# Performance work log

Hardware: AMD Instinct MI355X
Metric: run time of the kernel (lower is better)

The kernel has to match this reference:

```python
import jax, jax.numpy as jnp
import numpy as np

ANGLE_BINS = 16
RADIUS_BINS = 8


def _bilinear_cart(img, ys, xs):
    # img [B,C,H,W]; ys/xs: sample grid [A,R] in pixel coords, zero outside image
    h, w = img.shape[2], img.shape[3]
    y0 = jnp.floor(ys)
    x0 = jnp.floor(xs)
    wy = (ys - y0).astype(img.dtype)
    wx = (xs - x0).astype(img.dtype)
    y0i = jnp.clip(y0, 0, h - 1).astype(jnp.int32)
    y1i = jnp.clip(y0 + 1, 0, h - 1).astype(jnp.int32)
    x0i = jnp.clip(x0, 0, w - 1).astype(jnp.int32)
    x1i = jnp.clip(x0 + 1, 0, w - 1).astype(jnp.int32)
    v00 = img[:, :, y0i, x0i]
    v01 = img[:, :, y0i, x1i]
    v10 = img[:, :, y1i, x0i]
    v11 = img[:, :, y1i, x1i]
    out = (v00 * (1 - wy) * (1 - wx) + v01 * (1 - wy) * wx
           + v10 * wy * (1 - wx) + v11 * wy * wx)
    valid = ((ys >= 0) & (ys <= h - 1) & (xs >= 0) & (xs <= w - 1)).astype(img.dtype)
    return out * valid


def cartesian_to_polar(x):
    # [B,C,H,W] -> [B,C,ANGLE_BINS,RADIUS_BINS] via bilinear sampling on a polar grid
    b, c, h, w = x.shape
    cy = (h - 1) / 2.0
    cx = (w - 1) / 2.0
    max_r = min(h, w) / 2.0
    theta = 2.0 * jnp.pi * jnp.arange(ANGLE_BINS, dtype=jnp.float32) / ANGLE_BINS
    r = (jnp.arange(RADIUS_BINS, dtype=jnp.float32) + 0.5) / RADIUS_BINS * max_r
    ys = cy + r[None, :] * jnp.sin(theta)[:, None]  # [A,R]
    xs = cx + r[None, :] * jnp.cos(theta)[:, None]  # [A,R]
    return _bilinear_cart(x, ys, xs)


def polar_to_cartesian(pf, h, w):
    # [B,C,A,R] -> [B,C,H,W]: inverse remap with angular wrap, radial clamp,
    # zero outside the max radius disc
    b, c, A, R = pf.shape
    cy = (h - 1) / 2.0
    cx = (w - 1) / 2.0
    max_r = min(h, w) / 2.0
    yy, xx = jnp.meshgrid(jnp.arange(h, dtype=jnp.float32),
                          jnp.arange(w, dtype=jnp.float32), indexing='ij')
    dy = yy - cy
    dx = xx - cx
    rr = jnp.sqrt(dy * dy + dx * dx)
    th = jnp.mod(jnp.arctan2(dy, dx), 2.0 * jnp.pi)
    a = th / (2.0 * jnp.pi) * A
    ri = rr / max_r * R - 0.5
    a0 = jnp.floor(a)
    wa = (a - a0).astype(pf.dtype)
    a0i = jnp.mod(a0.astype(jnp.int32), A)
    a1i = jnp.mod(a0i + 1, A)
    r0 = jnp.floor(ri)
    wr = (ri - r0).astype(pf.dtype)
    r0i = jnp.clip(r0, 0, R - 1).astype(jnp.int32)
    r1i = jnp.clip(r0 + 1, 0, R - 1).astype(jnp.int32)
    v00 = pf[:, :, a0i, r0i]
    v01 = pf[:, :, a0i, r1i]
    v10 = pf[:, :, a1i, r0i]
    v11 = pf[:, :, a1i, r1i]
    out = (v00 * (1 - wa) * (1 - wr) + v01 * (1 - wa) * wr
           + v10 * wa * (1 - wr) + v11 * wa * wr)
    valid = (rr <= max_r).astype(pf.dtype)
    return out * valid


def setup_inputs() -> dict:
    key = jax.random.key(0)
    ks = jax.random.split(key, 4)
    B, C, H, W = 16, 256, 128, 128
    x = jax.random.normal(ks[0], (B, C, H, W), dtype=jnp.float32)
    # grouped 3x3 conv: groups=4 -> kernel [C_out=C, C_in/groups=C//4, 3, 3]
    w_polar = jax.random.normal(ks[1], (C, C // 4, 3, 3), dtype=jnp.float32) * 0.05
    b_polar = jnp.zeros((C,), jnp.float32)
    w_attn1 = jax.random.normal(ks[2], (C // 4, C), dtype=jnp.float32) * 0.05
    b_attn1 = jnp.zeros((C // 4,), jnp.float32)
    w_attn2 = jax.random.normal(ks[3], (1, C // 4), dtype=jnp.float32) * 0.05
    b_attn2 = jnp.zeros((1,), jnp.float32)
    return {"x": x, "w_polar": w_polar, "b_polar": b_polar,
            "w_attn1": w_attn1, "b_attn1": b_attn1,
            "w_attn2": w_attn2, "b_attn2": b_attn2}


def reference(x, w_polar, b_polar, w_attn1, b_attn1, w_attn2, b_attn2):
    b, c, h, w = x.shape
    pf = cartesian_to_polar(x)  # [B,C,16,8]
    pp = jax.lax.conv_general_dilated(
        pf, w_polar, window_strides=(1, 1), padding=((1, 1), (1, 1)),
        dimension_numbers=('NCHW', 'OIHW', 'NCHW'), feature_group_count=4)
    pp = pp + b_polar[None, :, None, None]
    pc = polar_to_cartesian(pp, h, w)  # [B,C,H,W]
    h1 = jax.nn.relu(jnp.einsum('bchw,oc->bohw', pc, w_attn1)
                     + b_attn1[None, :, None, None])
    att = jax.nn.sigmoid(jnp.einsum('bchw,oc->bohw', h1, w_attn2)
                         + b_attn2[None, :, None, None])  # [B,1,H,W]
    return x * att
```

## Files before the change

kernel.cpp:

```cpp
#include <hip/hip_runtime.h>
#include <math.h>

#define TWO_PI 6.28318530717958647692f

typedef float f4 __attribute__((ext_vector_type(4)));

__global__ __launch_bounds__(256) void k1_cart2polar(const float* __restrict__ x,
                                                     float* __restrict__ pf) {
    __shared__ float w00s[128], w01s[128], w10s[128], w11s[128];
    __shared__ int   o00s[128], o01s[128], o10s[128], o11s[128];
    int tid = threadIdx.x;
    if (tid < 128) {
        int a = tid >> 3, r = tid & 7;
        float theta = (TWO_PI * (float)a) / 16.0f;
        float rad   = ((float)r + 0.5f) / 8.0f * 64.0f;
        float ys = 63.5f + rad * sinf(theta);
        float xs = 63.5f + rad * cosf(theta);
        float y0 = floorf(ys), x0 = floorf(xs);
        float wy = ys - y0,    wx = xs - x0;
        int y0i = min(max((int)y0, 0), 127);
        int y1i = min(max((int)y0 + 1, 0), 127);
        int x0i = min(max((int)x0, 0), 127);
        int x1i = min(max((int)x0 + 1, 0), 127);
        float valid = (ys >= 0.0f && ys <= 127.0f && xs >= 0.0f && xs <= 127.0f) ? 1.0f : 0.0f;
        w00s[tid] = valid * (1.0f - wy) * (1.0f - wx);
        w01s[tid] = valid * (1.0f - wy) * wx;
        w10s[tid] = valid * wy * (1.0f - wx);
        w11s[tid] = valid * wy * wx;
        o00s[tid] = y0i * 128 + x0i;
        o01s[tid] = y0i * 128 + x1i;
        o10s[tid] = y1i * 128 + x0i;
        o11s[tid] = y1i * 128 + x1i;
    }
    __syncthreads();
    int t = blockIdx.x * 256 + tid;
    int bin = t & 127;
    int img = t >> 7;
    const float* ib = x + ((size_t)img << 14);
    float v = ib[o00s[bin]] * w00s[bin]
            + ib[o01s[bin]] * w01s[bin]
            + ib[o10s[bin]] * w10s[bin]
            + ib[o11s[bin]] * w11s[bin];
    pf[t] = v;
}

__global__ __launch_bounds__(256) void k2_conv(const float* __restrict__ pf,
                                               const float* __restrict__ w_polar,
                                               const float* __restrict__ b_polar,
                                               float* __restrict__ pp_t) {
    __shared__ __align__(16) float pfs[64 * 180];
    __shared__ __align__(16) float red[128 * 8];
    int bid = blockIdx.x;
    int b  = bid >> 5;
    int g  = (bid >> 3) & 3;
    int ot = bid & 7;
    int tid = threadIdx.x;
    for (int i = tid; i < 64 * 180; i += 256) pfs[i] = 0.0f;
    __syncthreads();
    const float* src = pf + ((size_t)(b * 256 + g * 64) << 7);
    for (int i = tid; i < 8192; i += 256) {
        int ic = i >> 7, bin = i & 127;
        pfs[ic * 180 + ((bin >> 3) + 1) * 10 + (bin & 7) + 1] = src[i];
    }
    __syncthreads();

    int half = tid >> 7;
    int bt   = tid & 127;
    int a = bt >> 3, r = bt & 7;
    int oc0 = g * 64 + ot * 8;
    float acc[8];
    #pragma unroll
    for (int j = 0; j < 8; ++j) acc[j] = 0.0f;

    const float* wbase = w_polar + (size_t)oc0 * 576 + half * 288;
    const float* pbase = pfs + half * 32 * 180 + a * 10 + r;
    for (int ic = 0; ic < 32; ++ic) {
        float v[9];
        const float* base = pbase + ic * 180;
        #pragma unroll
        for (int dh = 0; dh < 3; ++dh)
            #pragma unroll
            for (int dw = 0; dw < 3; ++dw)
                v[dh * 3 + dw] = base[dh * 10 + dw];
        #pragma unroll
        for (int j = 0; j < 8; ++j) {
            const float* wp = wbase + j * 576 + ic * 9;
            acc[j] += wp[0]*v[0] + wp[1]*v[1] + wp[2]*v[2]
                    + wp[3]*v[3] + wp[4]*v[4] + wp[5]*v[5]
                    + wp[6]*v[6] + wp[7]*v[7] + wp[8]*v[8];
        }
    }
    if (half) {
        #pragma unroll
        for (int j = 0; j < 8; ++j) red[bt * 8 + j] = acc[j];
    }
    __syncthreads();
    if (!half) {
        float* dst = pp_t + ((size_t)((b << 7) + bt)) * 256 + oc0;
        #pragma unroll
        for (int j = 0; j < 8; ++j)
            dst[j] = acc[j] + red[bt * 8 + j] + b_polar[oc0 + j];
    }
}

__global__ __launch_bounds__(256) void k3_proj(const float* __restrict__ pp_t,
                                               const float* __restrict__ w_attn1,
                                               float* __restrict__ q) {
    __shared__ __align__(16) float wl[16384];
    int tid = threadIdx.x;
    for (int i = tid; i < 16384; i += 256) {
        int o = i >> 8, c = i & 255;
        wl[(c << 6) + (o ^ (c & 31))] = w_attn1[i];
    }
    __syncthreads();
    int n = blockIdx.x * 256 + tid;
    int b   = n >> 13;
    int bin = (n >> 6) & 127;
    int o   = n & 63;
    const float4* pr4 = (const float4*)(pp_t + ((size_t)((b << 7) + bin)) * 256);
    float acc = 0.0f;
    #pragma unroll 8
    for (int c4 = 0; c4 < 64; ++c4) {
        float4 p = pr4[c4];
        int c = c4 << 2;
        acc += wl[( c      << 6) + (o ^ ( c      & 31))] * p.x;
        acc += wl[((c + 1) << 6) + (o ^ ((c + 1) & 31))] * p.y;
        acc += wl[((c + 2) << 6) + (o ^ ((c + 2) & 31))] * p.z;
        acc += wl[((c + 3) << 6) + (o ^ ((c + 3) & 31))] * p.w;
    }
    q[n] = acc;
}

__global__ __launch_bounds__(256) void k4a_att(const float* __restrict__ q,
                                               const float* __restrict__ b_attn1,
                                               const float* __restrict__ w_attn2,
                                               const float* __restrict__ b_attn2,
                                               float* __restrict__ att) {
    __shared__ __align__(16) float qs[8896];
    __shared__ __align__(16) float b1s[64];
    __shared__ __align__(16) float w2s[64];
    int b    = blockIdx.x >> 6;
    int tile = blockIdx.x & 63;
    int tid  = threadIdx.x;
    const float* qb = q + ((size_t)b << 13);
    for (int i = tid; i < 8192; i += 256) {
        int bin = i >> 6, o = i & 63;
        qs[(bin >> 3) * 556 + (bin & 7) * 68 + o] = qb[i];
    }
    if (tid < 64) { b1s[tid] = b_attn1[tid]; w2s[tid] = w_attn2[tid]; }
    __syncthreads();
    float b2 = b_attn2[0];
    const float4* q4  = (const float4*)qs;
    const float4* b14 = (const float4*)b1s;
    const float4* w24 = (const float4*)w2s;

    int p = (tile << 8) + tid;
    int h = p >> 7, w = p & 127;
    float dy = (float)h - 63.5f;
    float dx = (float)w - 63.5f;
    float rr = sqrtf(dy * dy + dx * dx);
    float th = atan2f(dy, dx);
    if (th < 0.0f) th += TWO_PI;
    float aa = th / TWO_PI * 16.0f;
    float a0 = floorf(aa);
    float wa = aa - a0;
    int ia0 = ((int)a0) & 15;
    int ia1 = (ia0 + 1) & 15;
    float ri = rr / 64.0f * 8.0f - 0.5f;
    float r0 = floorf(ri);
    float wr = ri - r0;
    int ir0 = (int)fminf(fmaxf(r0, 0.0f), 7.0f);
    int ir1 = (int)fminf(fmaxf(r0 + 1.0f, 0.0f), 7.0f);
    float valid = (rr <= 64.0f) ? 1.0f : 0.0f;
    float w00 = valid * (1.0f - wa) * (1.0f - wr);
    float w01 = valid * (1.0f - wa) * wr;
    float w10 = valid * wa * (1.0f - wr);
    float w11 = valid * wa * wr;
    int t00 = ia0 * 139 + ir0 * 17;
    int t01 = ia0 * 139 + ir1 * 17;
    int t10 = ia1 * 139 + ir0 * 17;
    int t11 = ia1 * 139 + ir1 * 17;
    float acc = b2;
    #pragma unroll
    for (int i = 0; i < 16; ++i) {
        float4 v00 = q4[t00 + i], v01 = q4[t01 + i];
        float4 v10 = q4[t10 + i], v11 = q4[t11 + i];
        float4 bb = b14[i], ww = w24[i];
        float sx = w00 * v00.x + w01 * v01.x + w10 * v10.x + w11 * v11.x;
        float sy = w00 * v00.y + w01 * v01.y + w10 * v10.y + w11 * v11.y;
        float sz = w00 * v00.z + w01 * v01.z + w10 * v10.z + w11 * v11.z;
        float sw = w00 * v00.w + w01 * v01.w + w10 * v10.w + w11 * v11.w;
        acc += fmaxf(sx + bb.x, 0.0f) * ww.x;
        acc += fmaxf(sy + bb.y, 0.0f) * ww.y;
        acc += fmaxf(sz + bb.z, 0.0f) * ww.z;
        acc += fmaxf(sw + bb.w, 0.0f) * ww.w;
    }
    float attv = 1.0f / (1.0f + __expf(-acc));
    att[((size_t)b << 14) + p] = attv;
}

__global__ __launch_bounds__(256) void k4b_mul(const f4* __restrict__ x4,
                                               const float* __restrict__ att,
                                               f4* __restrict__ out4) {
    const f4* att4 = (const f4*)att;
    int idx = blockIdx.x * 256 + threadIdx.x;
    int stride = gridDim.x * 256;
    for (int i = idx; i < 16777216; i += stride) {
        f4 xv = __builtin_nontemporal_load(&x4[i]);
        f4 av = att4[((i >> 20) << 12) | (i & 4095)];
        __builtin_nontemporal_store(xv * av, &out4[i]);
    }
}

extern "C" void kernel_launch(void* const* d_in, const int* in_sizes, int n_in,
                              void* d_out, int out_size, void* d_ws, size_t ws_size,
                              hipStream_t stream) {
    const float* x       = (const float*)d_in[0];
    const float* w_polar = (const float*)d_in[1];
    const float* b_polar = (const float*)d_in[2];
    const float* w_attn1 = (const float*)d_in[3];
    const float* b_attn1 = (const float*)d_in[4];
    const float* w_attn2 = (const float*)d_in[5];
    const float* b_attn2 = (const float*)d_in[6];
    float* out = (float*)d_out;
    float* ws  = (float*)d_ws;

    float* pf   = ws;
    float* pp_t = ws + 524288;
    float* q    = ws + 1048576;
    float* att  = ws + 1179648;

    hipLaunchKernelGGL(k1_cart2polar, dim3(2048), dim3(256), 0, stream, x, pf);
    hipLaunchKernelGGL(k2_conv,       dim3(512),  dim3(256), 0, stream, pf, w_polar, b_polar, pp_t);
    hipLaunchKernelGGL(k3_proj,       dim3(512),  dim3(256), 0, stream, pp_t, w_attn1, q);
    hipLaunchKernelGGL(k4a_att,       dim3(1024), dim3(256), 0, stream, q, b_attn1, w_attn2, b_attn2, att);
    hipLaunchKernelGGL(k4b_mul,       dim3(4096), dim3(256), 0, stream,
                       (const f4*)x, att, (f4*)out);
}
```

Measured before the change: 176.6 us.

## Fuse all stages into one persistent kernel with software grid barriers

Merges the five stage kernels into a single persistent kernel of 256 blocks. Stages are separated by an atomic-counter grid barrier, and each block covers several of the old blocks' work per stage. The aim is to remove the launch gaps and tail drain between the small kernels. The cost is far fewer resident blocks (256 blocks of 256 threads) for the bandwidth-bound final multiply, plus spin-barrier overhead and a memset. The barrier also relies on all 256 blocks being co-resident, which is not guaranteed without a cooperative launch.

```diff
diff --git a/kernel.cpp b/kernel.cpp
--- a/kernel.cpp
+++ b/kernel.cpp
@@ -5,210 +5,240 @@
 
 typedef float f4 __attribute__((ext_vector_type(4)));
 
-__global__ __launch_bounds__(256) void k1_cart2polar(const float* __restrict__ x,
-                                                     float* __restrict__ pf) {
-    __shared__ float w00s[128], w01s[128], w10s[128], w11s[128];
-    __shared__ int   o00s[128], o01s[128], o10s[128], o11s[128];
+#define NBLK 256u
+
+__device__ __forceinline__ void gbar(unsigned* cnt, unsigned target) {
+    __syncthreads();
+    __threadfence();
+    if (threadIdx.x == 0) {
+        atomicAdd(cnt, 1u);
+        while (__hip_atomic_load(cnt, __ATOMIC_ACQUIRE,
+                                 __HIP_MEMORY_SCOPE_AGENT) < target)
+            __builtin_amdgcn_s_sleep(4);
+    }
+    __syncthreads();
+    __threadfence();
+}
+
+__global__ __launch_bounds__(256, 2) void mega(
+        const float* __restrict__ x,
+        const float* __restrict__ w_polar,
+        const float* __restrict__ b_polar,
+        const float* __restrict__ w_attn1,
+        const float* __restrict__ b_attn1,
+        const float* __restrict__ w_attn2,
+        const float* __restrict__ b_attn2,
+        float* __restrict__ pf,
+        float* __restrict__ pp_t,
+        float* __restrict__ q,
+        float* __restrict__ att,
+        float* __restrict__ out,
+        unsigned* __restrict__ barcnt) {
+    __shared__ __align__(16) float sp[16384];
     int tid = threadIdx.x;
-    if (tid < 128) {
-        int a = tid >> 3, r = tid & 7;
-        float theta = (TWO_PI * (float)a) / 16.0f;
-        float rad   = ((float)r + 0.5f) / 8.0f * 64.0f;
-        float ys = 63.5f + rad * sinf(theta);
-        float xs = 63.5f + rad * cosf(theta);
-        float y0 = floorf(ys), x0 = floorf(xs);
-        float wy = ys - y0,    wx = xs - x0;
-        int y0i = min(max((int)y0, 0), 127);
-        int y1i = min(max((int)y0 + 1, 0), 127);
-        int x0i = min(max((int)x0, 0), 127);
-        int x1i = min(max((int)x0 + 1, 0), 127);
-        float valid = (ys >= 0.0f && ys <= 127.0f && xs >= 0.0f && xs <= 127.0f) ? 1.0f : 0.0f;
-        w00s[tid] = valid * (1.0f - wy) * (1.0f - wx);
-        w01s[tid] = valid * (1.0f - wy) * wx;
-        w10s[tid] = valid * wy * (1.0f - wx);
-        w11s[tid] = valid * wy * wx;
-        o00s[tid] = y0i * 128 + x0i;
-        o01s[tid] = y0i * 128 + x1i;
-        o10s[tid] = y1i * 128 + x0i;
-        o11s[tid] = y1i * 128 + x1i;
-    }
-    __syncthreads();
-    int t = blockIdx.x * 256 + tid;
-    int bin = t & 127;
-    int img = t >> 7;
-    const float* ib = x + ((size_t)img << 14);
-    float v = ib[o00s[bin]] * w00s[bin]
-            + ib[o01s[bin]] * w01s[bin]
-            + ib[o10s[bin]] * w10s[bin]
-            + ib[o11s[bin]] * w11s[bin];
-    pf[t] = v;
-}
-
-__global__ __launch_bounds__(256) void k2_conv(const float* __restrict__ pf,
-                                               const float* __restrict__ w_polar,
-                                               const float* __restrict__ b_polar,
-                                               float* __restrict__ pp_t) {
-    __shared__ __align__(16) float pfs[64 * 180];
-    __shared__ __align__(16) float red[128 * 8];
-    int bid = blockIdx.x;
-    int b  = bid >> 5;
-    int g  = (bid >> 3) & 3;
-    int ot = bid & 7;
-    int tid = threadIdx.x;
-    for (int i = tid; i < 64 * 180; i += 256) pfs[i] = 0.0f;
-    __syncthreads();
-    const float* src = pf + ((size_t)(b * 256 + g * 64) << 7);
-    for (int i = tid; i < 8192; i += 256) {
-        int ic = i >> 7, bin = i & 127;
-        pfs[ic * 180 + ((bin >> 3) + 1) * 10 + (bin & 7) + 1] = src[i];
-    }
-    __syncthreads();
-
-    int half = tid >> 7;
-    int bt   = tid & 127;
-    int a = bt >> 3, r = bt & 7;
-    int oc0 = g * 64 + ot * 8;
-    float acc[8];
-    #pragma unroll
-    for (int j = 0; j < 8; ++j) acc[j] = 0.0f;
-
-    const float* wbase = w_polar + (size_t)oc0 * 576 + half * 288;
-    const float* pbase = pfs + half * 32 * 180 + a * 10 + r;
-    for (int ic = 0; ic < 32; ++ic) {
-        float v[9];
-        const float* base = pbase + ic * 180;
-        #pragma unroll
-        for (int dh = 0; dh < 3; ++dh)
-            #pragma unroll
-            for (int dw = 0; dw < 3; ++dw)
-                v[dh * 3 + dw] = base[dh * 10 + dw];
+    int blk = blockIdx.x;
+
+    {
+        float* w00s = sp;        float* w01s = sp + 128;
+        float* w10s = sp + 256;  float* w11s = sp + 384;
+        int*   o00s = (int*)(sp + 512);  int* o01s = (int*)(sp + 640);
+        int*   o10s = (int*)(sp + 768);  int* o11s = (int*)(sp + 896);
+        if (tid < 128) {
+            int a = tid >> 3, r = tid & 7;
+            float theta = (TWO_PI * (float)a) / 16.0f;
+            float rad   = ((float)r + 0.5f) / 8.0f * 64.0f;
+            float ys = 63.5f + rad * sinf(theta);
+            float xs = 63.5f + rad * cosf(theta);
+            float y0 = floorf(ys), x0 = floorf(xs);
+            float wy = ys - y0,    wx = xs - x0;
+            int y0i = min(max((int)y0, 0), 127);
+            int y1i = min(max((int)y0 + 1, 0), 127);
+            int x0i = min(max((int)x0, 0), 127);
+            int x1i = min(max((int)x0 + 1, 0), 127);
+            float valid = (ys >= 0.0f && ys <= 127.0f && xs >= 0.0f && xs <= 127.0f) ? 1.0f : 0.0f;
+            w00s[tid] = valid * (1.0f - wy) * (1.0f - wx);
+            w01s[tid] = valid * (1.0f - wy) * wx;
+            w10s[tid] = valid * wy * (1.0f - wx);
+            w11s[tid] = valid * wy * wx;
+            o00s[tid] = y0i * 128 + x0i;
+            o01s[tid] = y0i * 128 + x1i;
+            o10s[tid] = y1i * 128 + x0i;
+            o11s[tid] = y1i * 128 + x1i;
+        }
+        __syncthreads();
+        int bin = tid & 127;
+        float W0 = w00s[bin], W1 = w01s[bin], W2 = w10s[bin], W3 = w11s[bin];
+        int O0 = o00s[bin], O1 = o01s[bin], O2 = o10s[bin], O3 = o11s[bin];
         #pragma unroll
         for (int j = 0; j < 8; ++j) {
-            const float* wp = wbase + j * 576 + ic * 9;
-            acc[j] += wp[0]*v[0] + wp[1]*v[1] + wp[2]*v[2]
-                    + wp[3]*v[3] + wp[4]*v[4] + wp[5]*v[5]
-                    + wp[6]*v[6] + wp[7]*v[7] + wp[8]*v[8];
-        }
-    }
-    if (half) {
+            int t = blk * 2048 + j * 256 + tid;
+            int img = t >> 7;
+            const float* ib = x + ((size_t)img << 14);
+            pf[t] = ib[O0] * W0 + ib[O1] * W1 + ib[O2] * W2 + ib[O3] * W3;
+        }
+    }
+    gbar(barcnt, 1 * NBLK);
+
+    {
+        float* pfs = sp;
+        float* red = sp + 11520;
+        for (int i = tid; i < 64 * 180; i += 256) pfs[i] = 0.0f;
+        for (int rep = 0; rep < 2; ++rep) {
+            int role = (blk << 1) | rep;
+            int b  = role >> 5;
+            int g  = (role >> 3) & 3;
+            int ot = role & 7;
+            __syncthreads();
+            const float* src = pf + ((size_t)(b * 256 + g * 64) << 7);
+            for (int i = tid; i < 8192; i += 256) {
+                int ic = i >> 7, bin = i & 127;
+                pfs[ic * 180 + ((bin >> 3) + 1) * 10 + (bin & 7) + 1] = src[i];
+            }
+            __syncthreads();
+            int half = tid >> 7;
+            int bt   = tid & 127;
+            int a = bt >> 3, r = bt & 7;
+            int oc0 = g * 64 + ot * 8;
+            float acc[8];
+            #pragma unroll
+            for (int j = 0; j < 8; ++j) acc[j] = 0.0f;
+            const float* wbase = w_polar + (size_t)oc0 * 576 + half * 288;
+            const float* pbase = pfs + half * 32 * 180 + a * 10 + r;
+            for (int ic = 0; ic < 32; ++ic) {
+                float v[9];
+                const float* base = pbase + ic * 180;
+                #pragma unroll
+                for (int dh = 0; dh < 3; ++dh)
+                    #pragma unroll
+                    for (int dw = 0; dw < 3; ++dw)
+                        v[dh * 3 + dw] = base[dh * 10 + dw];
+                #pragma unroll
+                for (int j = 0; j < 8; ++j) {
+                    const float* wp = wbase + j * 576 + ic * 9;
+                    acc[j] += wp[0]*v[0] + wp[1]*v[1] + wp[2]*v[2]
+                            + wp[3]*v[3] + wp[4]*v[4] + wp[5]*v[5]
+                            + wp[6]*v[6] + wp[7]*v[7] + wp[8]*v[8];
+                }
+            }
+            if (half) {
+                #pragma unroll
+                for (int j = 0; j < 8; ++j) red[bt * 8 + j] = acc[j];
+            }
+            __syncthreads();
+            if (!half) {
+                float* dst = pp_t + ((size_t)((b << 7) + bt)) * 256 + oc0;
+                #pragma unroll
+                for (int j = 0; j < 8; ++j)
+                    dst[j] = acc[j] + red[bt * 8 + j] + b_polar[oc0 + j];
+            }
+        }
+    }
+    gbar(barcnt, 2 * NBLK);
+
+    {
+        float* wl = sp;
+        for (int i = tid; i < 16384; i += 256) {
+            int o = i >> 8, c = i & 255;
+            wl[(c << 6) + (o ^ (c & 31))] = w_attn1[i];
+        }
+        __syncthreads();
         #pragma unroll
-        for (int j = 0; j < 8; ++j) red[bt * 8 + j] = acc[j];
-    }
-    __syncthreads();
-    if (!half) {
-        float* dst = pp_t + ((size_t)((b << 7) + bt)) * 256 + oc0;
+        for (int rep = 0; rep < 2; ++rep) {
+            int n = blk * 512 + rep * 256 + tid;
+            int b   = n >> 13;
+            int bin = (n >> 6) & 127;
+            int o   = n & 63;
+            const float4* pr4 = (const float4*)(pp_t + ((size_t)((b << 7) + bin)) * 256);
+            float acc = 0.0f;
+            #pragma unroll 8
+            for (int c4 = 0; c4 < 64; ++c4) {
+                float4 p = pr4[c4];
+                int c = c4 << 2;
+                acc += wl[( c      << 6) + (o ^ ( c      & 31))] * p.x;
+                acc += wl[((c + 1) << 6) + (o ^ ((c + 1) & 31))] * p.y;
+                acc += wl[((c + 2) << 6) + (o ^ ((c + 2) & 31))] * p.z;
+                acc += wl[((c + 3) << 6) + (o ^ ((c + 3) & 31))] * p.w;
+            }
+            q[n] = acc;
+        }
+    }
+    gbar(barcnt, 3 * NBLK);
+
+    {
+        float* qs  = sp;
+        float* b1s = sp + 8896;
+        float* w2s = sp + 8960;
+        int b       = blk >> 4;
+        int quarter = blk & 15;
+        const float* qb = q + ((size_t)b << 13);
+        for (int i = tid; i < 8192; i += 256) {
+            int bin = i >> 6, o = i & 63;
+            qs[(bin >> 3) * 556 + (bin & 7) * 68 + o] = qb[i];
+        }
+        if (tid < 64) { b1s[tid] = b_attn1[tid]; w2s[tid] = w_attn2[tid]; }
+        __syncthreads();
+        float b2 = b_attn2[0];
+        const float4* q4  = (const float4*)qs;
+        const float4* b14 = (const float4*)b1s;
+        const float4* w24 = (const float4*)w2s;
         #pragma unroll
-        for (int j = 0; j < 8; ++j)
-            dst[j] = acc[j] + red[bt * 8 + j] + b_polar[oc0 + j];
-    }
-}
-
-__global__ __launch_bounds__(256) void k3_proj(const float* __restrict__ pp_t,
-                                               const float* __restrict__ w_attn1,
-                                               float* __restrict__ q) {
-    __shared__ __align__(16) float wl[16384];
-    int tid = threadIdx.x;
-    for (int i = tid; i < 16384; i += 256) {
-        int o = i >> 8, c = i & 255;
-        wl[(c << 6) + (o ^ (c & 31))] = w_attn1[i];
-    }
-    __syncthreads();
-    int n = blockIdx.x * 256 + tid;
-    int b   = n >> 13;
-    int bin = (n >> 6) & 127;
-    int o   = n & 63;
-    const float4* pr4 = (const float4*)(pp_t + ((size_t)((b << 7) + bin)) * 256);
-    float acc = 0.0f;
-    #pragma unroll 8
-    for (int c4 = 0; c4 < 64; ++c4) {
-        float4 p = pr4[c4];
-        int c = c4 << 2;
-        acc += wl[( c      << 6) + (o ^ ( c      & 31))] * p.x;
-        acc += wl[((c + 1) << 6) + (o ^ ((c + 1) & 31))] * p.y;
-        acc += wl[((c + 2) << 6) + (o ^ ((c + 2) & 31))] * p.z;
-        acc += wl[((c + 3) << 6) + (o ^ ((c + 3) & 31))] * p.w;
-    }
-    q[n] = acc;
-}
-
-__global__ __launch_bounds__(256) void k4a_att(const float* __restrict__ q,
-                                               const float* __restrict__ b_attn1,
-                                               const float* __restrict__ w_attn2,
-                                               const float* __restrict__ b_attn2,
-                                               float* __restrict__ att) {
-    __shared__ __align__(16) float qs[8896];
-    __shared__ __align__(16) float b1s[64];
-    __shared__ __align__(16) float w2s[64];
-    int b    = blockIdx.x >> 6;
-    int tile = blockIdx.x & 63;
-    int tid  = threadIdx.x;
-    const float* qb = q + ((size_t)b << 13);
-    for (int i = tid; i < 8192; i += 256) {
-        int bin = i >> 6, o = i & 63;
-        qs[(bin >> 3) * 556 + (bin & 7) * 68 + o] = qb[i];
-    }
-    if (tid < 64) { b1s[tid] = b_attn1[tid]; w2s[tid] = w_attn2[tid]; }
-    __syncthreads();
-    float b2 = b_attn2[0];
-    const float4* q4  = (const float4*)qs;
-    const float4* b14 = (const float4*)b1s;
-    const float4* w24 = (const float4*)w2s;
-
-    int p = (tile << 8) + tid;
-    int h = p >> 7, w = p & 127;
-    float dy = (float)h - 63.5f;
-    float dx = (float)w - 63.5f;
-    float rr = sqrtf(dy * dy + dx * dx);
-    float th = atan2f(dy, dx);
-    if (th < 0.0f) th += TWO_PI;
-    float aa = th / TWO_PI * 16.0f;
-    float a0 = floorf(aa);
-    float wa = aa - a0;
-    int ia0 = ((int)a0) & 15;
-    int ia1 = (ia0 + 1) & 15;
-    float ri = rr / 64.0f * 8.0f - 0.5f;
-    float r0 = floorf(ri);
-    float wr = ri - r0;
-    int ir0 = (int)fminf(fmaxf(r0, 0.0f), 7.0f);
-    int ir1 = (int)fminf(fmaxf(r0 + 1.0f, 0.0f), 7.0f);
-    float valid = (rr <= 64.0f) ? 1.0f : 0.0f;
-    float w00 = valid * (1.0f - wa) * (1.0f - wr);
-    float w01 = valid * (1.0f - wa) * wr;
-    float w10 = valid * wa * (1.0f - wr);
-    float w11 = valid * wa * wr;
-    int t00 = ia0 * 139 + ir0 * 17;
-    int t01 = ia0 * 139 + ir1 * 17;
-    int t10 = ia1 * 139 + ir0 * 17;
-    int t11 = ia1 * 139 + ir1 * 17;
-    float acc = b2;
-    #pragma unroll
-    for (int i = 0; i < 16; ++i) {
-        float4 v00 = q4[t00 + i], v01 = q4[t01 + i];
-        float4 v10 = q4[t10 + i], v11 = q4[t11 + i];
-        float4 bb = b14[i], ww = w24[i];
-        float sx = w00 * v00.x + w01 * v01.x + w10 * v10.x + w11 * v11.x;
-        float sy = w00 * v00.y + w01 * v01.y + w10 * v10.y + w11 * v11.y;
-        float sz = w00 * v00.z + w01 * v01.z + w10 * v10.z + w11 * v11.z;
-        float sw = w00 * v00.w + w01 * v01.w + w10 * v10.w + w11 * v11.w;
-        acc += fmaxf(sx + bb.x, 0.0f) * ww.x;
-        acc += fmaxf(sy + bb.y, 0.0f) * ww.y;
-        acc += fmaxf(sz + bb.z, 0.0f) * ww.z;
-        acc += fmaxf(sw + bb.w, 0.0f) * ww.w;
-    }
-    float attv = 1.0f / (1.0f + __expf(-acc));
-    att[((size_t)b << 14) + p] = attv;
-}
-
-__global__ __launch_bounds__(256) void k4b_mul(const f4* __restrict__ x4,
-                                               const float* __restrict__ att,
-                                               f4* __restrict__ out4) {
-    const f4* att4 = (const f4*)att;
-    int idx = blockIdx.x * 256 + threadIdx.x;
-    int stride = gridDim.x * 256;
-    for (int i = idx; i < 16777216; i += stride) {
-        f4 xv = __builtin_nontemporal_load(&x4[i]);
-        f4 av = att4[((i >> 20) << 12) | (i & 4095)];
-        __builtin_nontemporal_store(xv * av, &out4[i]);
+        for (int k = 0; k < 4; ++k) {
+            int p = (quarter << 10) + (k << 8) + tid;
+            int h = p >> 7, w = p & 127;
+            float dy = (float)h - 63.5f;
+            float dx = (float)w - 63.5f;
+            float rr = sqrtf(dy * dy + dx * dx);
+            float th = atan2f(dy, dx);
+            if (th < 0.0f) th += TWO_PI;
+            float aa = th / TWO_PI * 16.0f;
+            float a0 = floorf(aa);
+            float wa = aa - a0;
+            int ia0 = ((int)a0) & 15;
+            int ia1 = (ia0 + 1) & 15;
+            float ri = rr / 64.0f * 8.0f - 0.5f;
+            float r0 = floorf(ri);
+            float wr = ri - r0;
+            int ir0 = (int)fminf(fmaxf(r0, 0.0f), 7.0f);
+            int ir1 = (int)fminf(fmaxf(r0 + 1.0f, 0.0f), 7.0f);
+            float valid = (rr <= 64.0f) ? 1.0f : 0.0f;
+            float w00 = valid * (1.0f - wa) * (1.0f - wr);
+            float w01 = valid * (1.0f - wa) * wr;
+            float w10 = valid * wa * (1.0f - wr);
+            float w11 = valid * wa * wr;
+            int t00 = ia0 * 139 + ir0 * 17;
+            int t01 = ia0 * 139 + ir1 * 17;
+            int t10 = ia1 * 139 + ir0 * 17;
+            int t11 = ia1 * 139 + ir1 * 17;
+            float acc = b2;
+            #pragma unroll
+            for (int i = 0; i < 16; ++i) {
+                float4 v00 = q4[t00 + i], v01 = q4[t01 + i];
+                float4 v10 = q4[t10 + i], v11 = q4[t11 + i];
+                float4 bb = b14[i], ww = w24[i];
+                float sx = w00 * v00.x + w01 * v01.x + w10 * v10.x + w11 * v11.x;
+                float sy = w00 * v00.y + w01 * v01.y + w10 * v10.y + w11 * v11.y;
+                float sz = w00 * v00.z + w01 * v01.z + w10 * v10.z + w11 * v11.z;
+                float sw = w00 * v00.w + w01 * v01.w + w10 * v10.w + w11 * v11.w;
+                acc += fmaxf(sx + bb.x, 0.0f) * ww.x;
+                acc += fmaxf(sy + bb.y, 0.0f) * ww.y;
+                acc += fmaxf(sz + bb.z, 0.0f) * ww.z;
+                acc += fmaxf(sw + bb.w, 0.0f) * ww.w;
+            }
+            att[((size_t)b << 14) + p] = 1.0f / (1.0f + __expf(-acc));
+        }
+    }
+    gbar(barcnt, 4 * NBLK);
+
+    {
+        const f4* x4   = (const f4*)x;
+        const f4* att4 = (const f4*)att;
+        f4* out4 = (f4*)out;
+        int idx = blk * 256 + tid;
+        for (int i = idx; i < 16777216; i += 65536) {
+            f4 xv = __builtin_nontemporal_load(&x4[i]);
+            f4 av = att4[((i >> 20) << 12) | (i & 4095)];
+            __builtin_nontemporal_store(xv * av, &out4[i]);
+        }
     }
 }
 
@@ -225,15 +255,14 @@
     float* out = (float*)d_out;
     float* ws  = (float*)d_ws;
 
-    float* pf   = ws;
-    float* pp_t = ws + 524288;
-    float* q    = ws + 1048576;
-    float* att  = ws + 1179648;
-
-    hipLaunchKernelGGL(k1_cart2polar, dim3(2048), dim3(256), 0, stream, x, pf);
-    hipLaunchKernelGGL(k2_conv,       dim3(512),  dim3(256), 0, stream, pf, w_polar, b_polar, pp_t);
-    hipLaunchKernelGGL(k3_proj,       dim3(512),  dim3(256), 0, stream, pp_t, w_attn1, q);
-    hipLaunchKernelGGL(k4a_att,       dim3(1024), dim3(256), 0, stream, q, b_attn1, w_attn2, b_attn2, att);
-    hipLaunchKernelGGL(k4b_mul,       dim3(4096), dim3(256), 0, stream,
-                       (const f4*)x, att, (f4*)out);
+    float*    pf     = ws;
+    float*    pp_t   = ws + 524288;
+    float*    q      = ws + 1048576;
+    float*    att    = ws + 1179648;
+    unsigned* barcnt = (unsigned*)(ws + 1572864);
+
+    hipMemsetAsync((void*)barcnt, 0, 64, stream);
+    hipLaunchKernelGGL(mega, dim3(NBLK), dim3(256), 0, stream,
+                       x, w_polar, b_polar, w_attn1, b_attn1, w_attn2, b_attn2,
+                       pf, pp_t, q, att, out, barcnt);
 }
```

Result: slower. 471.4 us (+167.0%).

## Fuse cart-to-polar sampling into the grouped polar conv kernel

Applied to the files above, without the earlier changes.

Merges the bilinear cart-to-polar gather and the grouped 3x3 polar convolution into one kernel. It uses 64 blocks of 1024 threads, each computing one batch-group tile of all 64 output channels over the full 64 input channels. This removes a kernel launch, the pf workspace round trip and the cross-half reduction. The sampling also drops the clamping and validity mask, which is safe only because every sample point falls inside a 128x128 image. In exchange the conv stage runs on far fewer workgroups with a longer per-thread loop, and the final multiply launch is halved in grid size.

```diff
diff --git a/kernel.cpp b/kernel.cpp
--- a/kernel.cpp
+++ b/kernel.cpp
@@ -5,76 +5,55 @@
 
 typedef float f4 __attribute__((ext_vector_type(4)));
 
-__global__ __launch_bounds__(256) void k1_cart2polar(const float* __restrict__ x,
-                                                     float* __restrict__ pf) {
-    __shared__ float w00s[128], w01s[128], w10s[128], w11s[128];
-    __shared__ int   o00s[128], o01s[128], o10s[128], o11s[128];
+__global__ __launch_bounds__(1024, 1) void k12_fused(const float* __restrict__ x,
+                                                     const float* __restrict__ w_polar,
+                                                     const float* __restrict__ b_polar,
+                                                     float* __restrict__ pp_t) {
+    __shared__ float w0s[128], w1s[128], w2s[128], w3s[128];
+    __shared__ int   o0s[128];
+    __shared__ __align__(16) float pfs[64 * 180];
     int tid = threadIdx.x;
+    int b = blockIdx.x >> 2;
+    int g = blockIdx.x & 3;
+
     if (tid < 128) {
         int a = tid >> 3, r = tid & 7;
         float theta = (TWO_PI * (float)a) / 16.0f;
-        float rad   = ((float)r + 0.5f) / 8.0f * 64.0f;
+        float rad   = ((float)r + 0.5f) * 8.0f;
         float ys = 63.5f + rad * sinf(theta);
         float xs = 63.5f + rad * cosf(theta);
         float y0 = floorf(ys), x0 = floorf(xs);
         float wy = ys - y0,    wx = xs - x0;
-        int y0i = min(max((int)y0, 0), 127);
-        int y1i = min(max((int)y0 + 1, 0), 127);
-        int x0i = min(max((int)x0, 0), 127);
-        int x1i = min(max((int)x0 + 1, 0), 127);
-        float valid = (ys >= 0.0f && ys <= 127.0f && xs >= 0.0f && xs <= 127.0f) ? 1.0f : 0.0f;
-        w00s[tid] = valid * (1.0f - wy) * (1.0f - wx);
-        w01s[tid] = valid * (1.0f - wy) * wx;
-        w10s[tid] = valid * wy * (1.0f - wx);
-        w11s[tid] = valid * wy * wx;
-        o00s[tid] = y0i * 128 + x0i;
-        o01s[tid] = y0i * 128 + x1i;
-        o10s[tid] = y1i * 128 + x0i;
-        o11s[tid] = y1i * 128 + x1i;
-    }
-    __syncthreads();
-    int t = blockIdx.x * 256 + tid;
-    int bin = t & 127;
-    int img = t >> 7;
-    const float* ib = x + ((size_t)img << 14);
-    float v = ib[o00s[bin]] * w00s[bin]
-            + ib[o01s[bin]] * w01s[bin]
-            + ib[o10s[bin]] * w10s[bin]
-            + ib[o11s[bin]] * w11s[bin];
-    pf[t] = v;
-}
-
-__global__ __launch_bounds__(256) void k2_conv(const float* __restrict__ pf,
-                                               const float* __restrict__ w_polar,
-                                               const float* __restrict__ b_polar,
-                                               float* __restrict__ pp_t) {
-    __shared__ __align__(16) float pfs[64 * 180];
-    __shared__ __align__(16) float red[128 * 8];
-    int bid = blockIdx.x;
-    int b  = bid >> 5;
-    int g  = (bid >> 3) & 3;
-    int ot = bid & 7;
-    int tid = threadIdx.x;
-    for (int i = tid; i < 64 * 180; i += 256) pfs[i] = 0.0f;
-    __syncthreads();
-    const float* src = pf + ((size_t)(b * 256 + g * 64) << 7);
-    for (int i = tid; i < 8192; i += 256) {
+        w0s[tid] = (1.0f - wy) * (1.0f - wx);
+        w1s[tid] = (1.0f - wy) * wx;
+        w2s[tid] = wy * (1.0f - wx);
+        w3s[tid] = wy * wx;
+        o0s[tid] = (int)y0 * 128 + (int)x0;
+    }
+    for (int i = tid; i < 64 * 180; i += 1024) pfs[i] = 0.0f;
+    __syncthreads();
+
+    for (int i = tid; i < 8192; i += 1024) {
         int ic = i >> 7, bin = i & 127;
-        pfs[ic * 180 + ((bin >> 3) + 1) * 10 + (bin & 7) + 1] = src[i];
-    }
-    __syncthreads();
-
-    int half = tid >> 7;
+        const float* ib = x + ((size_t)(b * 256 + g * 64 + ic) << 14);
+        int o = o0s[bin];
+        float v = ib[o]       * w0s[bin] + ib[o + 1]   * w1s[bin]
+                + ib[o + 128] * w2s[bin] + ib[o + 129] * w3s[bin];
+        pfs[ic * 180 + ((bin >> 3) + 1) * 10 + (bin & 7) + 1] = v;
+    }
+    __syncthreads();
+
+    int slot = tid >> 7;
     int bt   = tid & 127;
     int a = bt >> 3, r = bt & 7;
-    int oc0 = g * 64 + ot * 8;
+    int oc0 = g * 64 + slot * 8;
     float acc[8];
     #pragma unroll
     for (int j = 0; j < 8; ++j) acc[j] = 0.0f;
 
-    const float* wbase = w_polar + (size_t)oc0 * 576 + half * 288;
-    const float* pbase = pfs + half * 32 * 180 + a * 10 + r;
-    for (int ic = 0; ic < 32; ++ic) {
+    const float* wbase = w_polar + (size_t)oc0 * 576;
+    const float* pbase = pfs + a * 10 + r;
+    for (int ic = 0; ic < 64; ++ic) {
         float v[9];
         const float* base = pbase + ic * 180;
         #pragma unroll
@@ -90,17 +69,9 @@
                     + wp[6]*v[6] + wp[7]*v[7] + wp[8]*v[8];
         }
     }
-    if (half) {
-        #pragma unroll
-        for (int j = 0; j < 8; ++j) red[bt * 8 + j] = acc[j];
-    }
-    __syncthreads();
-    if (!half) {
-        float* dst = pp_t + ((size_t)((b << 7) + bt)) * 256 + oc0;
-        #pragma unroll
-        for (int j = 0; j < 8; ++j)
-            dst[j] = acc[j] + red[bt * 8 + j] + b_polar[oc0 + j];
-    }
+    float* dst = pp_t + ((size_t)(b * 128 + bt)) * 256 + oc0;
+    #pragma unroll
+    for (int j = 0; j < 8; ++j) dst[j] = acc[j] + b_polar[oc0 + j];
 }
 
 __global__ __launch_bounds__(256) void k3_proj(const float* __restrict__ pp_t,
@@ -225,15 +196,15 @@
     float* out = (float*)d_out;
     float* ws  = (float*)d_ws;
 
-    float* pf   = ws;
-    float* pp_t = ws + 524288;
-    float* q    = ws + 1048576;
-    float* att  = ws + 1179648;
-
-    hipLaunchKernelGGL(k1_cart2polar, dim3(2048), dim3(256), 0, stream, x, pf);
-    hipLaunchKernelGGL(k2_conv,       dim3(512),  dim3(256), 0, stream, pf, w_polar, b_polar, pp_t);
-    hipLaunchKernelGGL(k3_proj,       dim3(512),  dim3(256), 0, stream, pp_t, w_attn1, q);
-    hipLaunchKernelGGL(k4a_att,       dim3(1024), dim3(256), 0, stream, q, b_attn1, w_attn2, b_attn2, att);
-    hipLaunchKernelGGL(k4b_mul,       dim3(4096), dim3(256), 0, stream,
+    float* pp_t = ws;
+    float* q    = ws + 524288;
+    float* att  = ws + 655360;
+
+    hipLaunchKernelGGL(k12_fused, dim3(64),   dim3(1024), 0, stream,
+                       x, w_polar, b_polar, pp_t);
+    hipLaunchKernelGGL(k3_proj,   dim3(512),  dim3(256), 0, stream, pp_t, w_attn1, q);
+    hipLaunchKernelGGL(k4a_att,   dim3(1024), dim3(256), 0, stream,
+                       q, b_attn1, w_attn2, b_attn2, att);
+    hipLaunchKernelGGL(k4b_mul,   dim3(2048), dim3(256), 0, stream,
                        (const f4*)x, att, (f4*)out);
 }
```

New measurement: 281.8 us. 59.6% more time.
